# Performance work log

Measured on AMD Instinct MI355X. Metric: run time of the kernel, lower is better.

The kernel has to match this reference:

```python
import jax, jax.numpy as jnp
import numpy as np
import math

D_MODEL = 2048
N_HEAD = 16
D_HEAD = D_MODEL // N_HEAD
B, T = 4, 2048


def bitlinear(x, w):
    # gamma: global abs-mean scale of the weight, clamped
    gamma = jnp.maximum(jnp.mean(jnp.abs(w)), 1e-5)
    w_quant = jnp.clip(jnp.round(w / gamma), -1.0, 1.0)
    # straight-through estimator: forward uses ternary weights, grad flows to w
    w_eff = jax.lax.stop_gradient(w_quant - w) + w
    return jnp.matmul(x, w_eff.T) * gamma


def setup_inputs() -> dict:
    key = jax.random.key(0)
    kx, kq, kk, kv, ko = jax.random.split(key, 5)
    s = 0.02
    return {
        "x": jax.random.normal(kx, (B, T, D_MODEL), dtype=jnp.float32),
        "wq": jax.random.normal(kq, (D_MODEL, D_MODEL), dtype=jnp.float32) * s,
        "wk": jax.random.normal(kk, (D_MODEL, D_MODEL), dtype=jnp.float32) * s,
        "wv": jax.random.normal(kv, (D_MODEL, D_MODEL), dtype=jnp.float32) * s,
        "wo": jax.random.normal(ko, (D_MODEL, D_MODEL), dtype=jnp.float32) * s,
    }


def reference(x, wq, wk, wv, wo):
    b, t, c = x.shape
    # BitLinear QKV projections -> (B, H, T, Dh)
    def split_heads(y):
        return y.reshape(b, t, N_HEAD, D_HEAD).transpose(0, 2, 1, 3)

    q = split_heads(bitlinear(x, wq))
    k = split_heads(bitlinear(x, wk))
    v = split_heads(bitlinear(x, wv))

    scale = 1.0 / math.sqrt(D_HEAD)
    scores = jnp.einsum("bhqd,bhkd->bhqk", q, k) * scale  # (B,H,T,T)
    causal = jnp.tril(jnp.ones((t, t), dtype=bool))
    scores = jnp.where(causal, scores, jnp.finfo(scores.dtype).min)
    attn = jax.nn.softmax(scores, axis=-1)
    out = jnp.einsum("bhqk,bhkd->bhqd", attn, v)  # (B,H,T,Dh)
    out = out.transpose(0, 2, 1, 3).reshape(b, t, c)
    return bitlinear(out, wo)
```

## Files before the change

### kernel.cpp

```cpp
#include <hip/hip_runtime.h>
#include <stdint.h>

#define D_MODEL 2048
#define NHEAD   16
#define DHEAD   128
#define BATCH   4
#define SEQ     2048
#define MROWS   (BATCH*SEQ)
#define WELEMS  (D_MODEL*D_MODEL)
#define NITEMS  2048

typedef __attribute__((ext_vector_type(4))) float          f32x4;
typedef __attribute__((ext_vector_type(8))) short          s16x8;
typedef __attribute__((ext_vector_type(4))) unsigned short u16x4;

__device__ __forceinline__ unsigned short f2bf(float f) {
  union { float f; uint32_t u; } v; v.f = f;
  uint32_t r = v.u + 0x7fffu + ((v.u >> 16) & 1u);
  return (unsigned short)(r >> 16);
}

__device__ __forceinline__ void load_lds16(const void* g, void* l) {
  __builtin_amdgcn_global_load_lds(
      (__attribute__((address_space(1))) void*)(g),
      (__attribute__((address_space(3))) void*)(l), 16, 0, 0);
}

__device__ __forceinline__ float gamma_of(const double* sums, int gidx) {
  double gs = sums[gidx] * (1.0 / (double)WELEMS);
  if (gs < 1e-5) gs = 1e-5;
  return (float)gs;
}

__global__ __launch_bounds__(256) void absmean_kernel(
    const float* __restrict__ w0, const float* __restrict__ w1,
    const float* __restrict__ w2, const float* __restrict__ w3,
    double* __restrict__ sums) {
  const float* w = blockIdx.y == 0 ? w0 : blockIdx.y == 1 ? w1
                 : blockIdx.y == 2 ? w2 : w3;
  double acc = 0.0;
  const int stride = gridDim.x * blockDim.x;
  for (int i = blockIdx.x * blockDim.x + threadIdx.x; i < WELEMS / 4; i += stride) {
    float4 v = ((const float4*)w)[i];
    acc += (double)fabsf(v.x) + (double)fabsf(v.y) +
           (double)fabsf(v.z) + (double)fabsf(v.w);
  }
  acc += __shfl_xor(acc, 1);  acc += __shfl_xor(acc, 2);  acc += __shfl_xor(acc, 4);
  acc += __shfl_xor(acc, 8);  acc += __shfl_xor(acc, 16); acc += __shfl_xor(acc, 32);
  __shared__ double wsum[4];
  const int lane = threadIdx.x & 63, wave = threadIdx.x >> 6;
  if (lane == 0) wsum[wave] = acc;
  __syncthreads();
  if (threadIdx.x == 0)
    atomicAdd(&sums[blockIdx.y], wsum[0] + wsum[1] + wsum[2] + wsum[3]);
}

__global__ __launch_bounds__(256) void quant_kernel(
    const float* __restrict__ wsrc, unsigned short* __restrict__ wt,
    const double* __restrict__ sums, int gidx) {
  const float gf = gamma_of(sums, gidx);
  const int i = blockIdx.x * 256 + threadIdx.x;
  float4 v = ((const float4*)wsrc)[i];
  u16x4 r;
  r[0] = f2bf(fminf(1.f, fmaxf(-1.f, rintf(v.x / gf))));
  r[1] = f2bf(fminf(1.f, fmaxf(-1.f, rintf(v.y / gf))));
  r[2] = f2bf(fminf(1.f, fmaxf(-1.f, rintf(v.z / gf))));
  r[3] = f2bf(fminf(1.f, fmaxf(-1.f, rintf(v.w / gf))));
  ((u16x4*)wt)[i] = r;
}

__global__ __launch_bounds__(256) void cvt_bf16_kernel(
    const float* __restrict__ x, unsigned short* __restrict__ xb) {
  const int i = blockIdx.x * 256 + threadIdx.x;
  float4 v = ((const float4*)x)[i];
  u16x4 r;
  r[0] = f2bf(v.x); r[1] = f2bf(v.y); r[2] = f2bf(v.z); r[3] = f2bf(v.w);
  ((u16x4*)xb)[i] = r;
}

template <int MODE>
__global__ __launch_bounds__(512, 2) void gemm_bt_kernel(
    const unsigned short* __restrict__ A,
    const unsigned short* __restrict__ Bt,
    void* __restrict__ out,
    const double* __restrict__ sums, int gidx, float escale) {
  constexpr int K = D_MODEL;
  constexpr int NT = K / 32;
  extern __shared__ char smem[];

  const int tid = threadIdx.x, lane = tid & 63, wave = tid >> 6;
  const int g = lane >> 4, r15 = lane & 15;
  const int wm = wave >> 2, wn = wave & 3;

  const int wgid = (blockIdx.x & 7) * 32 + (blockIdx.x >> 3);
  const int rowBase = (wgid >> 3) * 256, colBase = (wgid & 7) * 256;

  const int o0 = tid * 16, o1 = 8192 + tid * 16;
  const int sr0 = o0 >> 6, sc0 = (o0 & 63) ^ ((sr0 & 3) << 4);
  const int sr1 = o1 >> 6, sc1 = (o1 & 63) ^ ((sr1 & 3) << 4);
  const unsigned short* ApS0 = A  + (size_t)(rowBase + sr0) * K + (sc0 >> 1);
  const unsigned short* ApS1 = A  + (size_t)(rowBase + sr1) * K + (sc1 >> 1);
  const unsigned short* BpS0 = Bt + (size_t)(colBase + sr0) * K + (sc0 >> 1);
  const unsigned short* BpS1 = Bt + (size_t)(colBase + sr1) * K + (sc1 >> 1);

  char* b0 = smem; char* b1 = smem + 32768; char* b2 = smem + 65536;
  const int woff = wave * 1024;

  const int sw = (g * 16) ^ ((r15 & 3) << 4);
  const int arow = wm * 128 + r15;
  const int brow = wn * 64 + r15;

  f32x4 acc[8][4] = {};

  load_lds16(ApS0, b0 + woff);          load_lds16(ApS1, b0 + 8192 + woff);
  load_lds16(BpS0, b0 + 16384 + woff);  load_lds16(BpS1, b0 + 24576 + woff);
  load_lds16(ApS0 + 32, b1 + woff);         load_lds16(ApS1 + 32, b1 + 8192 + woff);
  load_lds16(BpS0 + 32, b1 + 16384 + woff); load_lds16(BpS1 + 32, b1 + 24576 + woff);
  asm volatile("s_waitcnt vmcnt(4)" ::: "memory");
  __builtin_amdgcn_sched_barrier(0);
  __builtin_amdgcn_s_barrier();
  __builtin_amdgcn_sched_barrier(0);

#pragma unroll 1
  for (int t = 0; t < NT; ++t) {
    const bool pf = (t + 2 < NT);
    const int koff = (t + 2) * 32;

    if (pf) {
      load_lds16(ApS0 + koff, b2 + woff);
      load_lds16(ApS1 + koff, b2 + 8192 + woff);
    }
    s16x8 bf[4], af[4];
#pragma unroll
    for (int fn = 0; fn < 4; ++fn)
      bf[fn] = *(const s16x8*)(b0 + 16384 + (brow + fn * 16) * 64 + sw);
#pragma unroll
    for (int fr = 0; fr < 4; ++fr)
      af[fr] = *(const s16x8*)(b0 + (arow + fr * 16) * 64 + sw);
    __builtin_amdgcn_s_setprio(1);
#pragma unroll
    for (int fr = 0; fr < 4; ++fr)
#pragma unroll
      for (int fn = 0; fn < 4; ++fn)
        acc[fr][fn] = __builtin_amdgcn_mfma_f32_16x16x32_bf16(af[fr], bf[fn], acc[fr][fn], 0, 0, 0);
    __builtin_amdgcn_s_setprio(0);

    if (pf) {
      load_lds16(BpS0 + koff, b2 + 16384 + woff);
      load_lds16(BpS1 + koff, b2 + 24576 + woff);
    }
#pragma unroll
    for (int fr = 0; fr < 4; ++fr)
      af[fr] = *(const s16x8*)(b0 + (arow + (fr + 4) * 16) * 64 + sw);
    __builtin_amdgcn_s_setprio(1);
#pragma unroll
    for (int fr = 0; fr < 4; ++fr)
#pragma unroll
      for (int fn = 0; fn < 4; ++fn)
        acc[fr + 4][fn] = __builtin_amdgcn_mfma_f32_16x16x32_bf16(af[fr], bf[fn], acc[fr + 4][fn], 0, 0, 0);
    __builtin_amdgcn_s_setprio(0);

    if (pf) asm volatile("s_waitcnt vmcnt(4)" ::: "memory");
    else    asm volatile("s_waitcnt vmcnt(0)" ::: "memory");
    __builtin_amdgcn_sched_barrier(0);
    __builtin_amdgcn_s_barrier();
    __builtin_amdgcn_sched_barrier(0);
    char* tmp = b0; b0 = b1; b1 = b2; b2 = tmp;
  }

  const float scale = gamma_of(sums, gidx) * escale;
#pragma unroll
  for (int fr = 0; fr < 8; ++fr) {
    const int row0 = rowBase + wm * 128 + fr * 16 + g * 4;
#pragma unroll
    for (int fn = 0; fn < 4; ++fn) {
      const int col = colBase + wn * 64 + fn * 16 + r15;
      if constexpr (MODE == 2) {
        float* op = (float*)out;
#pragma unroll
        for (int j = 0; j < 4; ++j)
          op[(size_t)(row0 + j) * D_MODEL + col] = acc[fr][fn][j] * scale;
      } else if constexpr (MODE == 0) {
        unsigned short* op = (unsigned short*)out;
#pragma unroll
        for (int j = 0; j < 4; ++j)
          op[(size_t)(row0 + j) * D_MODEL + col] = f2bf(acc[fr][fn][j] * scale);
      } else {
        unsigned short* op = (unsigned short*)out;
        const int bb = row0 >> 11, tt = row0 & 2047;
        const int hh = col >> 7,  d = col & 127;
        u16x4 r;
#pragma unroll
        for (int j = 0; j < 4; ++j) r[j] = f2bf(acc[fr][fn][j] * scale);
        *(u16x4*)(op + (((size_t)bb * NHEAD + hh) * DHEAD + d) * SEQ + tt) = r;
      }
    }
  }
}

__global__ __launch_bounds__(256, 4) void attn_kernel(
    const unsigned short* __restrict__ qg,
    const unsigned short* __restrict__ kg,
    const unsigned short* __restrict__ vtg,
    unsigned short* __restrict__ og,
    int* __restrict__ counter) {
  __shared__ unsigned short Ks[64 * 128];
  __shared__ unsigned short Vts[128 * 64];
  __shared__ unsigned short Ps[4][1024];
  __shared__ int s_item;

  const int tid = threadIdx.x, lane = tid & 63, wave = tid >> 6;
  const int g = lane >> 4, r15 = lane & 15;

  char* KsB = (char*)Ks; char* VtsB = (char*)Vts; char* PsB = (char*)(Ps[wave]);

  for (;;) {
    if (tid == 0) s_item = atomicAdd(counter, 1);
    __syncthreads();
    const int item = s_item;
    __syncthreads();
    if (item >= NITEMS) break;

    const int qs = 31 - (item >> 6);
    const int bh = item & 63;
    const int b = bh >> 4, h = bh & 15;

    const unsigned short* kbase = kg + (size_t)b * SEQ * D_MODEL + h * DHEAD;
    const unsigned short* vbase = vtg + (size_t)(b * NHEAD + h) * DHEAD * SEQ;

    s16x8 qf[4];
    {
      const unsigned short* qbase =
          qg + (size_t)(b * SEQ + qs * 64 + wave * 16 + r15) * D_MODEL + h * DHEAD;
#pragma unroll
      for (int c = 0; c < 4; ++c) qf[c] = *(const s16x8*)(qbase + c * 32 + g * 8);
    }

    f32x4 oacc[8] = {};
    float mr[4], lr[4];
#pragma unroll
    for (int j = 0; j < 4; ++j) { mr[j] = -1e30f; lr[j] = 0.f; }

    const int nt = qs + 1;

#pragma unroll 1
    for (int t = 0; t < nt; ++t) {
#pragma unroll
      for (int rnd = 0; rnd < 4; ++rnd) {
        const int ob = rnd * 4096 + wave * 1024 + lane * 16;
        const int krow = ob >> 8;
        const int ks = (ob & 255) ^ ((krow & 7) << 4);
        load_lds16(kbase + (size_t)(t * 64 + krow) * D_MODEL + (ks >> 1),
                   KsB + rnd * 4096 + wave * 1024);
        const int drow = ob >> 7;
        const int vs = (ob & 127) ^ ((drow & 7) << 4);
        load_lds16(vbase + (size_t)drow * SEQ + t * 64 + (vs >> 1),
                   VtsB + rnd * 4096 + wave * 1024);
      }
      __syncthreads();

      f32x4 s[4] = {};
      __builtin_amdgcn_s_setprio(1);
#pragma unroll
      for (int c = 0; c < 4; ++c) {
#pragma unroll
        for (int n = 0; n < 4; ++n) {
          const int key = n * 16 + r15;
          const int baddr = (((key << 8) | (c << 6) | (g << 4))) ^ ((key & 7) << 4);
          s16x8 kf = *(const s16x8*)(KsB + baddr);
          s[n] = __builtin_amdgcn_mfma_f32_16x16x32_bf16(qf[c], kf, s[n], 0, 0, 0);
        }
      }
      __builtin_amdgcn_s_setprio(0);

      if (t == qs) {
        const int q0 = qs * 64 + wave * 16 + g * 4;
        const int k0 = t * 64 + r15;
#pragma unroll
        for (int n = 0; n < 4; ++n)
#pragma unroll
          for (int j = 0; j < 4; ++j)
            if (k0 + n * 16 > q0 + j) s[n][j] = -1e30f;
      }
      float pm[4];
#pragma unroll
      for (int j = 0; j < 4; ++j)
        pm[j] = fmaxf(fmaxf(s[0][j], s[1][j]), fmaxf(s[2][j], s[3][j]));
#pragma unroll
      for (int j = 0; j < 4; ++j) {
        pm[j] = fmaxf(pm[j], __shfl_xor(pm[j], 1));
        pm[j] = fmaxf(pm[j], __shfl_xor(pm[j], 2));
        pm[j] = fmaxf(pm[j], __shfl_xor(pm[j], 4));
        pm[j] = fmaxf(pm[j], __shfl_xor(pm[j], 8));
      }
      bool ok = pm[0] <= mr[0] + 8.f && pm[1] <= mr[1] + 8.f &&
                pm[2] <= mr[2] + 8.f && pm[3] <= mr[3] + 8.f;
      if (!__all(ok)) {
#pragma unroll
        for (int j = 0; j < 4; ++j) {
          const float mn = fmaxf(mr[j], pm[j]);
          const float rf = exp2f(mr[j] - mn);
          mr[j] = mn;
          lr[j] *= rf;
#pragma unroll
          for (int n2 = 0; n2 < 8; ++n2) oacc[n2][j] *= rf;
        }
      }
      float psum[4] = {0.f, 0.f, 0.f, 0.f};
#pragma unroll
      for (int n = 0; n < 4; ++n) {
        const int keyl = n * 16 + r15;
#pragma unroll
        for (int j = 0; j < 4; ++j) {
          const float p = exp2f(s[n][j] - mr[j]);
          psum[j] += p;
          const int row = g * 4 + j;
          const int baddr = ((row << 7) | (keyl << 1)) ^ ((row & 7) << 4);
          *(unsigned short*)(PsB + baddr) = f2bf(p);
        }
      }
#pragma unroll
      for (int j = 0; j < 4; ++j) {
        psum[j] += __shfl_xor(psum[j], 1);
        psum[j] += __shfl_xor(psum[j], 2);
        psum[j] += __shfl_xor(psum[j], 4);
        psum[j] += __shfl_xor(psum[j], 8);
        lr[j] += psum[j];
      }
      __builtin_amdgcn_s_setprio(1);
#pragma unroll
      for (int c2 = 0; c2 < 2; ++c2) {
        const int baddr_p = (((r15 << 7) | (c2 << 6) | (g << 4))) ^ ((r15 & 7) << 4);
        s16x8 pa = *(const s16x8*)(PsB + baddr_p);
#pragma unroll
        for (int n2 = 0; n2 < 8; ++n2) {
          const int d = n2 * 16 + r15;
          const int baddr_v = (((d << 7) | (c2 << 6) | (g << 4))) ^ ((d & 7) << 4);
          s16x8 vf = *(const s16x8*)(VtsB + baddr_v);
          oacc[n2] = __builtin_amdgcn_mfma_f32_16x16x32_bf16(pa, vf, oacc[n2], 0, 0, 0);
        }
      }
      __builtin_amdgcn_s_setprio(0);
      __syncthreads();
    }

    unsigned short* obase =
        og + (size_t)(b * SEQ + qs * 64 + wave * 16 + g * 4) * D_MODEL + h * DHEAD;
    float inv[4];
#pragma unroll
    for (int j = 0; j < 4; ++j) inv[j] = 1.f / lr[j];
#pragma unroll
    for (int n2 = 0; n2 < 8; ++n2) {
      const int d = n2 * 16 + r15;
#pragma unroll
      for (int j = 0; j < 4; ++j)
        obase[(size_t)j * D_MODEL + d] = f2bf(oacc[n2][j] * inv[j]);
    }
  }
}

extern "C" void kernel_launch(void* const* d_in, const int* in_sizes, int n_in,
                              void* d_out, int out_size, void* d_ws, size_t ws_size,
                              hipStream_t stream) {
  const float* x  = (const float*)d_in[0];
  const float* wq = (const float*)d_in[1];
  const float* wk = (const float*)d_in[2];
  const float* wv = (const float*)d_in[3];
  const float* wo = (const float*)d_in[4];
  float* out = (float*)d_out;

  char* ws = (char*)d_ws;
  double* sums = (double*)ws;
  int* cnt = (int*)(ws + 64);
  size_t off = 256;
  unsigned short* wtern = (unsigned short*)(ws + off); off += (size_t)WELEMS * 2;
  unsigned short* xbf   = (unsigned short*)(ws + off); off += (size_t)MROWS * D_MODEL * 2;
  unsigned short* qb    = (unsigned short*)(ws + off); off += (size_t)MROWS * D_MODEL * 2;
  unsigned short* kb    = (unsigned short*)(ws + off); off += (size_t)MROWS * D_MODEL * 2;
  unsigned short* vtb   = (unsigned short*)(ws + off); off += (size_t)MROWS * D_MODEL * 2;
  unsigned short* attn_out = xbf;

  hipMemsetAsync(ws, 0, 256, stream);
  absmean_kernel<<<dim3(256, 4), 256, 0, stream>>>(wq, wk, wv, wo, sums);
  cvt_bf16_kernel<<<MROWS * D_MODEL / 4 / 256, 256, 0, stream>>>(x, xbf);

  const float qfold = 0.08838834764831845f * 1.4426950408889634f;

  const int ggrid = (MROWS / 256) * (D_MODEL / 256);
  const int glds = 98304;
  quant_kernel<<<WELEMS / 4 / 256, 256, 0, stream>>>(wq, wtern, sums, 0);
  gemm_bt_kernel<0><<<ggrid, 512, glds, stream>>>(xbf, wtern, qb, sums, 0, qfold);
  quant_kernel<<<WELEMS / 4 / 256, 256, 0, stream>>>(wk, wtern, sums, 1);
  gemm_bt_kernel<0><<<ggrid, 512, glds, stream>>>(xbf, wtern, kb, sums, 1, 1.0f);
  quant_kernel<<<WELEMS / 4 / 256, 256, 0, stream>>>(wv, wtern, sums, 2);
  gemm_bt_kernel<1><<<ggrid, 512, glds, stream>>>(xbf, wtern, vtb, sums, 2, 1.0f);

  attn_kernel<<<dim3(1024), 256, 0, stream>>>(qb, kb, vtb, attn_out, cnt);

  quant_kernel<<<WELEMS / 4 / 256, 256, 0, stream>>>(wo, wtern, sums, 3);
  gemm_bt_kernel<2><<<ggrid, 512, glds, stream>>>(attn_out, wtern, out, sums, 3, 1.0f);
}
```

Before: 633.8 us.

## Restructure GEMM mainloop into 8-phase ping-pong with K=64 tiles and staggered staging

The bf16 GEMM mainloop changes from a three-buffer K=32 pipeline to a two-buffer K=64 scheme split into eight phases per iteration. Each phase loads A fragments, issues a partial stage of the next tile's global-to-LDS loads, then runs a block of MFMAs bracketed by barriers. The aim is to spread memory traffic across compute phases and halve the number of main-loop iterations. In exchange it uses 128 KB of LDS per block instead of 96 KB, which at two blocks per CU may reduce occupancy, and it adds many extra workgroup barriers.

Result: faster. 613.0 us (-3.3%).

```diff
diff --git a/kernel.cpp b/kernel.cpp
--- a/kernel.cpp
+++ b/kernel.cpp
@@ -78,6 +78,50 @@
   ((u16x4*)xb)[i] = r;
 }
 
+#define NOSTAGE {}
+#define WAIT4 { asm volatile("s_waitcnt vmcnt(4)" ::: "memory"); __builtin_amdgcn_sched_barrier(0); }
+#define WAIT0 { asm volatile("s_waitcnt vmcnt(0)" ::: "memory"); __builtin_amdgcn_sched_barrier(0); }
+
+#define STAGE_OP(gptr, baseRow, t, h, d, bofs)                                       \
+  if ((t) < NT) {                                                                    \
+    load_lds16(gptr + (size_t)((baseRow) + (h)*128 + sr) * K + (t)*64 + sce,         \
+               smem + (bofs) + (d)*32768 + (h)*16384 + wave*1024);                   \
+    load_lds16(gptr + (size_t)((baseRow) + (h)*128 + 64 + sr) * K + (t)*64 + sce,    \
+               smem + (bofs) + (d)*32768 + (h)*16384 + 8192 + wave*1024);            \
+  }
+#define STAGE_A(t, h, d) STAGE_OP(A,  rowBase, t, h, d, 0)
+#define STAGE_B(t, h, d) STAGE_OP(Bt, colBase, t, h, d, 65536)
+
+#define PHASE(d, rb, FIRST, STAGES, WAITS)                                            \
+  {                                                                                   \
+    const char* Ab_ = smem + (d)*32768 + wm*16384;                                    \
+    s16x8 af[2][2];                                                                   \
+    _Pragma("unroll") for (int j = 0; j < 2; ++j)                                     \
+      _Pragma("unroll") for (int kc = 0; kc < 2; ++kc)                                \
+        af[j][kc] = *(const s16x8*)(Ab_ + (((rb)+j)*16 + r15)*128                     \
+                                    + (((kc<<6) | (g<<4)) ^ swz));                    \
+    if (FIRST) {                                                                      \
+      const char* Bb_ = smem + 65536 + (d)*32768 + (wn>>1)*16384;                     \
+      _Pragma("unroll") for (int fn = 0; fn < 4; ++fn)                                \
+        _Pragma("unroll") for (int kc = 0; kc < 2; ++kc)                              \
+          bfr[fn*2+kc] = *(const s16x8*)(Bb_ + ((wn&1)*64 + fn*16 + r15)*128          \
+                                         + (((kc<<6) | (g<<4)) ^ swz));               \
+    }                                                                                 \
+    STAGES;                                                                           \
+    __builtin_amdgcn_s_barrier();                                                     \
+    asm volatile("s_waitcnt lgkmcnt(0)" ::: "memory");                                \
+    __builtin_amdgcn_sched_barrier(0);                                                \
+    __builtin_amdgcn_s_setprio(1);                                                    \
+    _Pragma("unroll") for (int j = 0; j < 2; ++j)                                     \
+      _Pragma("unroll") for (int fn = 0; fn < 4; ++fn)                                \
+        _Pragma("unroll") for (int kc = 0; kc < 2; ++kc)                              \
+          acc[(rb)+j][fn] = __builtin_amdgcn_mfma_f32_16x16x32_bf16(                  \
+              af[j][kc], bfr[fn*2+kc], acc[(rb)+j][fn], 0, 0, 0);                     \
+    __builtin_amdgcn_s_setprio(0);                                                    \
+    WAITS;                                                                            \
+    __builtin_amdgcn_s_barrier();                                                     \
+  }
+
 template <int MODE>
 __global__ __launch_bounds__(512, 2) void gemm_bt_kernel(
     const unsigned short* __restrict__ A,
@@ -85,7 +129,7 @@
     void* __restrict__ out,
     const double* __restrict__ sums, int gidx, float escale) {
   constexpr int K = D_MODEL;
-  constexpr int NT = K / 32;
+  constexpr int NT = K / 64;
   extern __shared__ char smem[];
 
   const int tid = threadIdx.x, lane = tid & 63, wave = tid >> 6;
@@ -95,77 +139,34 @@
   const int wgid = (blockIdx.x & 7) * 32 + (blockIdx.x >> 3);
   const int rowBase = (wgid >> 3) * 256, colBase = (wgid & 7) * 256;
 
-  const int o0 = tid * 16, o1 = 8192 + tid * 16;
-  const int sr0 = o0 >> 6, sc0 = (o0 & 63) ^ ((sr0 & 3) << 4);
-  const int sr1 = o1 >> 6, sc1 = (o1 & 63) ^ ((sr1 & 3) << 4);
-  const unsigned short* ApS0 = A  + (size_t)(rowBase + sr0) * K + (sc0 >> 1);
-  const unsigned short* ApS1 = A  + (size_t)(rowBase + sr1) * K + (sc1 >> 1);
-  const unsigned short* BpS0 = Bt + (size_t)(colBase + sr0) * K + (sc0 >> 1);
-  const unsigned short* BpS1 = Bt + (size_t)(colBase + sr1) * K + (sc1 >> 1);
-
-  char* b0 = smem; char* b1 = smem + 32768; char* b2 = smem + 65536;
-  const int woff = wave * 1024;
-
-  const int sw = (g * 16) ^ ((r15 & 3) << 4);
-  const int arow = wm * 128 + r15;
-  const int brow = wn * 64 + r15;
+  const int sr = tid >> 3;
+  const int sce = ((((tid & 7) * 16) ^ ((sr & 7) << 4)) >> 1);
+  const int swz = (r15 & 7) << 4;
 
   f32x4 acc[8][4] = {};
-
-  load_lds16(ApS0, b0 + woff);          load_lds16(ApS1, b0 + 8192 + woff);
-  load_lds16(BpS0, b0 + 16384 + woff);  load_lds16(BpS1, b0 + 24576 + woff);
-  load_lds16(ApS0 + 32, b1 + woff);         load_lds16(ApS1 + 32, b1 + 8192 + woff);
-  load_lds16(BpS0 + 32, b1 + 16384 + woff); load_lds16(BpS1 + 32, b1 + 24576 + woff);
+  s16x8 bfr[8];
+
+  STAGE_B(0, 0, 0); STAGE_B(0, 1, 0);
+  STAGE_A(0, 0, 0); STAGE_A(0, 1, 0);
+  STAGE_B(1, 0, 1); STAGE_B(1, 1, 1);
   asm volatile("s_waitcnt vmcnt(4)" ::: "memory");
   __builtin_amdgcn_sched_barrier(0);
   __builtin_amdgcn_s_barrier();
-  __builtin_amdgcn_sched_barrier(0);
 
 #pragma unroll 1
-  for (int t = 0; t < NT; ++t) {
-    const bool pf = (t + 2 < NT);
-    const int koff = (t + 2) * 32;
-
-    if (pf) {
-      load_lds16(ApS0 + koff, b2 + woff);
-      load_lds16(ApS1 + koff, b2 + 8192 + woff);
-    }
-    s16x8 bf[4], af[4];
-#pragma unroll
-    for (int fn = 0; fn < 4; ++fn)
-      bf[fn] = *(const s16x8*)(b0 + 16384 + (brow + fn * 16) * 64 + sw);
-#pragma unroll
-    for (int fr = 0; fr < 4; ++fr)
-      af[fr] = *(const s16x8*)(b0 + (arow + fr * 16) * 64 + sw);
-    __builtin_amdgcn_s_setprio(1);
-#pragma unroll
-    for (int fr = 0; fr < 4; ++fr)
-#pragma unroll
-      for (int fn = 0; fn < 4; ++fn)
-        acc[fr][fn] = __builtin_amdgcn_mfma_f32_16x16x32_bf16(af[fr], bf[fn], acc[fr][fn], 0, 0, 0);
-    __builtin_amdgcn_s_setprio(0);
-
-    if (pf) {
-      load_lds16(BpS0 + koff, b2 + 16384 + woff);
-      load_lds16(BpS1 + koff, b2 + 24576 + woff);
-    }
-#pragma unroll
-    for (int fr = 0; fr < 4; ++fr)
-      af[fr] = *(const s16x8*)(b0 + (arow + (fr + 4) * 16) * 64 + sw);
-    __builtin_amdgcn_s_setprio(1);
-#pragma unroll
-    for (int fr = 0; fr < 4; ++fr)
-#pragma unroll
-      for (int fn = 0; fn < 4; ++fn)
-        acc[fr + 4][fn] = __builtin_amdgcn_mfma_f32_16x16x32_bf16(af[fr], bf[fn], acc[fr + 4][fn], 0, 0, 0);
-    __builtin_amdgcn_s_setprio(0);
-
-    if (pf) asm volatile("s_waitcnt vmcnt(4)" ::: "memory");
-    else    asm volatile("s_waitcnt vmcnt(0)" ::: "memory");
-    __builtin_amdgcn_sched_barrier(0);
-    __builtin_amdgcn_s_barrier();
-    __builtin_amdgcn_sched_barrier(0);
-    char* tmp = b0; b0 = b1; b1 = b2; b2 = tmp;
+  for (int it = 0; it < NT / 2; ++it) {
+    const int e = 2 * it;
+    const bool pf = (e + 2 < NT);
+    PHASE(0, 0, true,  STAGE_A(e+1, 0, 1), NOSTAGE);
+    PHASE(0, 2, false, STAGE_A(e+1, 1, 1), NOSTAGE);
+    PHASE(0, 4, false, STAGE_B(e+2, 0, 0), NOSTAGE);
+    if (pf) { PHASE(0, 6, false, STAGE_B(e+2, 1, 0), WAIT4); }
+    else    { PHASE(0, 6, false, NOSTAGE,            WAIT0); }
+    PHASE(1, 0, true,  STAGE_A(e+2, 0, 0), NOSTAGE);
+    PHASE(1, 2, false, STAGE_A(e+2, 1, 0), NOSTAGE);
+    PHASE(1, 4, false, STAGE_B(e+3, 0, 1), NOSTAGE);
+    if (pf) { PHASE(1, 6, false, STAGE_B(e+3, 1, 1), WAIT4); }
+    else    { PHASE(1, 6, false, NOSTAGE,            NOSTAGE); }
   }
 
   const float scale = gamma_of(sums, gidx) * escale;
@@ -387,7 +388,7 @@
   const float qfold = 0.08838834764831845f * 1.4426950408889634f;
 
   const int ggrid = (MROWS / 256) * (D_MODEL / 256);
-  const int glds = 98304;
+  const int glds = 131072;
   quant_kernel<<<WELEMS / 4 / 256, 256, 0, stream>>>(wq, wtern, sums, 0);
   gemm_bt_kernel<0><<<ggrid, 512, glds, stream>>>(xbf, wtern, qb, sums, 0, qfold);
   quant_kernel<<<WELEMS / 4 / 256, 256, 0, stream>>>(wk, wtern, sums, 1);
```
